# Optimization experiments

Measured on AMD Instinct MI355X. Metric: run time of the kernel, lower is better.

Reference implementation:

```python
import jax, jax.numpy as jnp
import numpy as np

N = 4096          # residues
D = 256           # local feature dim
FACTOR = 2
H = 8             # global heads
DF = D * FACTOR   # 512
DH = DF // H      # 64 per-head dim
NUM_CHAINS = 64
NUM_BATCHES = 8


def index_mean(x, idx, mask, num_segments):
    """Masked segment mean, gathered back to per-element shape.
    x: [N, ...], idx: [N] int, mask: broadcastable to x (0/1)."""
    m = mask.astype(x.dtype)
    xm = x * m
    s = jax.ops.segment_sum(xm, idx, num_segments=num_segments)
    c = jax.ops.segment_sum(jnp.broadcast_to(m, x.shape), idx, num_segments=num_segments)
    mean = s / jnp.maximum(c, 1e-6)
    return mean[idx]


def setup_inputs() -> dict:
    key = jax.random.key(0)
    ks = jax.random.split(key, 12)
    s_in = 1.0 / np.sqrt(D)
    s_mid = 1.0 / np.sqrt(2 * DF)
    return {
        "local": jax.random.normal(ks[0], (N, D), jnp.float32),
        "chain": jax.random.randint(ks[1], (N,), 0, NUM_CHAINS),
        "batch": jax.random.randint(ks[2], (N,), 0, NUM_BATCHES),
        "mask": jax.random.bernoulli(ks[3], 0.9, (N,)),
        "W_key": jax.random.normal(ks[4], (D, DF), jnp.float32) * s_in,
        "b_key": jnp.zeros((DF,), jnp.float32),
        "W_value": jax.random.normal(ks[5], (D, DF), jnp.float32) * s_in,
        "b_value": jnp.zeros((DF,), jnp.float32),
        "W_query": jax.random.normal(ks[6], (D, DF), jnp.float32) * s_in,
        "b_query": jnp.zeros((DF,), jnp.float32),
        "W_bias": jax.random.normal(ks[7], (D, 2 * DF), jnp.float32) * s_in,
        "b_bias": jnp.zeros((2 * DF,), jnp.float32),
        "W_out": jax.random.normal(ks[8], (2 * DF, D), jnp.float32) * s_mid,
    }


def reference(local, chain, batch, mask,
              W_key, b_key, W_value, b_value, W_query, b_query,
              W_bias, b_bias, W_out):
    n = local.shape[0]
    k = jax.nn.gelu(local @ W_key + b_key).reshape(n, H, DH)
    v = (local @ W_value + b_value).reshape(n, H, DH)
    q = jax.nn.gelu(local @ W_query + b_query).reshape(n, H, DH)

    bias = index_mean(local @ W_bias + b_bias, batch, mask[:, None], NUM_BATCHES)

    # outer product key (x) value: [N, H, DH, DH]
    ov = k[:, :, :, None] * v[:, :, None, :]
    m4 = mask[:, None, None, None]
    chain_op = index_mean(ov, chain, m4, NUM_CHAINS)
    batch_op = index_mean(ov, batch, m4, NUM_BATCHES)
    operation = jnp.concatenate((chain_op, batch_op), axis=-2)  # [N, H, 2*DH, DH]

    out = jnp.einsum('bhvk,bhk->bhv', operation, q).reshape(n, -1) + bias
    return out @ W_out
```

## Files before the change

kernel.cpp:

```cpp
#include <hip/hip_runtime.h>
#include <math.h>

#define NN 4096
#define DD 256
#define DFF 512
#define HH 8
#define DHH 64

#define CAP_C 256
#define CAP_B 1024

#define OFF_KB     0
#define OFF_VB     1048576
#define OFF_QB     2097152
#define OFF_ATTNB  3145728
#define OFF_STC    5242880
#define OFF_STB    7340032
#define OFF_LSUM   7602176
#define OFF_BSUM   7604224
#define OFF_CNT    7612416
#define OFF_LOCALB 7612672
#define OFF_WQKVT  8136960
#define OFF_WOUTT  8333568
#define OFF_LISTS  8464640
#define ZERO_BYTES ((OFF_LOCALB - OFF_STB) * 4)

typedef __attribute__((ext_vector_type(8))) short bf16x8;
typedef __attribute__((ext_vector_type(4))) float floatx4;

__device__ __forceinline__ float gelu_f(float x) {
    const float c = 0.7978845608028654f;
    float t = tanhf(c * (x + 0.044715f * x * x * x));
    return 0.5f * x * (1.0f + t);
}

__device__ __forceinline__ unsigned short f2b(float f) {
    union { float f; unsigned int u; } v; v.f = f;
    unsigned int r = (v.u + 0x7FFFu + ((v.u >> 16) & 1u)) >> 16;
    return (unsigned short)r;
}

__device__ __forceinline__ float b2f(unsigned short u) {
    union { unsigned int u; float f; } v; v.u = ((unsigned int)u) << 16;
    return v.f;
}

__global__ __launch_bounds__(256) void prep_kernel(
    const float* __restrict__ local,
    const float* __restrict__ Wk, const float* __restrict__ Wv,
    const float* __restrict__ Wq, const float* __restrict__ Wout,
    unsigned short* __restrict__ localb, unsigned short* __restrict__ Wqkvt,
    unsigned short* __restrict__ Woutt,
    const int* __restrict__ chain, const int* __restrict__ batch,
    const int* __restrict__ mask,
    int* __restrict__ cntc_m, int* __restrict__ cntc_all,
    int* __restrict__ cntb_m, int* __restrict__ cntb_all,
    int* __restrict__ listc_m, int* __restrict__ listc_all,
    int* __restrict__ listb_m, int* __restrict__ listb_all)
{
    const int bid = blockIdx.x, tid = threadIdx.x;
    if (bid < 1024) {
        int base = bid * 1024 + tid * 4;
        float4 v = *(const float4*)(local + base);
        ushort4 o;
        o.x = f2b(v.x); o.y = f2b(v.y); o.z = f2b(v.z); o.w = f2b(v.w);
        *(ushort4*)(localb + base) = o;
    } else if (bid < 1664) {
        int t = bid - 1024;
        const float* src; unsigned short* dst; int R, C, r0, c0;
        if (t < 384) {
            int m = t >> 7, ti = t & 127;
            src = (m == 0) ? Wk : (m == 1) ? Wv : Wq;
            dst = Wqkvt + (size_t)m * 512 * 256;
            R = 256; C = 512;
            r0 = (ti >> 4) * 32; c0 = (ti & 15) * 32;
        } else {
            int ti = t - 384;
            src = Wout; dst = Woutt;
            R = 1024; C = 256;
            r0 = (ti >> 3) * 32; c0 = (ti & 7) * 32;
        }
        __shared__ float Tl[32][33];
        int ty = tid >> 3, tx = tid & 7;
        float4 v = *(const float4*)(src + (size_t)(r0 + ty) * C + c0 + tx * 4);
        Tl[tx * 4 + 0][ty] = v.x;
        Tl[tx * 4 + 1][ty] = v.y;
        Tl[tx * 4 + 2][ty] = v.z;
        Tl[tx * 4 + 3][ty] = v.w;
        __syncthreads();
        int cy = tid >> 3, rx = tid & 7;
        ushort4 o;
        o.x = f2b(Tl[cy][rx * 4 + 0]);
        o.y = f2b(Tl[cy][rx * 4 + 1]);
        o.z = f2b(Tl[cy][rx * 4 + 2]);
        o.w = f2b(Tl[cy][rx * 4 + 3]);
        *(ushort4*)(dst + (size_t)(c0 + cy) * R + r0 + rx * 4) = o;
    } else {
        __shared__ int hc_m[64], hc_all[64], hb_m[8], hb_all[8];
        __shared__ int pc_m[64], pc_all[64], pb_m[8], pb_all[8];
        if (tid < 64) { hc_m[tid] = 0; hc_all[tid] = 0; }
        if (tid < 8)  { hb_m[tid] = 0; hb_all[tid] = 0; }
        __syncthreads();
        int n = (bid - 1664) * 256 + tid;
        int c = chain[n], b = batch[n], m = mask[n];
        int rc_all = atomicAdd(&hc_all[c], 1);
        int rb_all = atomicAdd(&hb_all[b], 1);
        int rc_m = -1, rb_m = -1;
        if (m) {
            rc_m = atomicAdd(&hc_m[c], 1);
            rb_m = atomicAdd(&hb_m[b], 1);
        }
        __syncthreads();
        if (tid < 64) {
            pc_all[tid] = atomicAdd(&cntc_all[tid], hc_all[tid]);
            pc_m[tid]   = atomicAdd(&cntc_m[tid],   hc_m[tid]);
        }
        if (tid < 8) {
            pb_all[tid] = atomicAdd(&cntb_all[tid], hb_all[tid]);
            pb_m[tid]   = atomicAdd(&cntb_m[tid],   hb_m[tid]);
        }
        __syncthreads();
        int ia = pc_all[c] + rc_all;
        if (ia < CAP_C) listc_all[c * CAP_C + ia] = n;
        int ib = pb_all[b] + rb_all;
        if (ib < CAP_B) listb_all[b * CAP_B + ib] = n;
        if (m) {
            int ja = pc_m[c] + rc_m;
            if (ja < CAP_C) listc_m[c * CAP_C + ja] = n;
            int jb = pb_m[b] + rb_m;
            if (jb < CAP_B) listb_m[b * CAP_B + jb] = n;
        }
    }
}

__global__ __launch_bounds__(256) void qkv_plus_kernel(
    const unsigned short* __restrict__ A, const unsigned short* __restrict__ Bt,
    const float* __restrict__ bk, const float* __restrict__ bv,
    const float* __restrict__ bq,
    unsigned short* __restrict__ KVQb,
    const float* __restrict__ local, const int* __restrict__ listb_m,
    const int* __restrict__ cntb_m, float* __restrict__ Lsum)
{
    const int tid = threadIdx.x;
    if (blockIdx.x == 12) {
        const int seg = blockIdx.y >> 2, z = blockIdx.y & 3;
        int c = min(cntb_m[seg], CAP_B);
        int chunk = (c + 3) / 4;
        int r0 = z * chunk, r1 = min(c, r0 + chunk);
        float acc = 0.0f;
        for (int g = r0; g < r1; ++g) {
            int n = listb_m[seg * CAP_B + g];
            acc += local[(size_t)n * DD + tid];
        }
        atomicAdd(&Lsum[seg * DD + tid], acc);
        return;
    }
    const int K = 256;
    __shared__ unsigned short Asl[128][72];
    __shared__ unsigned short Bsl[128][72];
    const int wave = tid >> 6, lane = tid & 63;
    const int kq = lane >> 4, la = lane & 15;
    const int row0 = blockIdx.y * 128, cg0 = blockIdx.x * 128;
    const int wrow = (wave & 1) * 64, wcol = (wave >> 1) * 64;

    floatx4 acc[4][4] = {};
    for (int kk = 0; kk < K; kk += 64) {
#pragma unroll
        for (int t = 0; t < 4; ++t) {
            int idx = tid + t * 256;
            int rr = idx >> 3, kc = (idx & 7) * 8;
            *(float4*)&Asl[rr][kc] = *(const float4*)(A + (size_t)(row0 + rr) * K + kk + kc);
            *(float4*)&Bsl[rr][kc] = *(const float4*)(Bt + (size_t)(cg0 + rr) * K + kk + kc);
        }
        __syncthreads();
#pragma unroll
        for (int ks = 0; ks < 2; ++ks) {
            bf16x8 af[4], bf[4];
#pragma unroll
            for (int t = 0; t < 4; ++t) {
                af[t] = *(const bf16x8*)&Asl[wrow + t * 16 + la][ks * 32 + kq * 8];
                bf[t] = *(const bf16x8*)&Bsl[wcol + t * 16 + la][ks * 32 + kq * 8];
            }
#pragma unroll
            for (int at = 0; at < 4; ++at)
#pragma unroll
                for (int ct = 0; ct < 4; ++ct)
                    acc[at][ct] = __builtin_amdgcn_mfma_f32_16x16x32_bf16(
                        af[at], bf[ct], acc[at][ct], 0, 0, 0);
        }
        __syncthreads();
    }
    const int sel = cg0 >> 9;
    const int do_gelu = (sel != 1);
    const float* bias = (sel == 0) ? bk : (sel == 1) ? bv : bq;
    unsigned short* C = KVQb + (size_t)sel * (NN * DFF);
#pragma unroll
    for (int ct = 0; ct < 4; ++ct) {
        int col = cg0 + wcol + ct * 16 + la;
        int colw = col & 511;
        float bb = bias[colw];
#pragma unroll
        for (int at = 0; at < 4; ++at) {
#pragma unroll
            for (int i = 0; i < 4; ++i) {
                int row = row0 + wrow + at * 16 + kq * 4 + i;
                float o = acc[at][ct][i] + bb;
                if (do_gelu) o = gelu_f(o);
                C[(size_t)row * DFF + colw] = f2b(o);
            }
        }
    }
}

__global__ __launch_bounds__(256) void mid_kernel(
    const unsigned short* __restrict__ Kb, const unsigned short* __restrict__ Vb,
    const int* __restrict__ listc_m, const int* __restrict__ cntc_m,
    float* __restrict__ STc,
    const int* __restrict__ listb_m, const int* __restrict__ cntb_m,
    float* __restrict__ STb,
    const float* __restrict__ Lsum, const float* __restrict__ W_bias,
    float* __restrict__ Bsum)
{
    const int id = blockIdx.x, tid = threadIdx.x;
    if (id >= 1024) {
        int t = id - 1024;
        const int seg = t >> 3, kz = t & 7;
        float4 acc = make_float4(0, 0, 0, 0);
        for (int k = kz * 32; k < kz * 32 + 32; ++k) {
            float l = Lsum[seg * DD + k];
            float4 w = *(const float4*)(W_bias + (size_t)k * 1024 + tid * 4);
            acc.x += l * w.x; acc.y += l * w.y; acc.z += l * w.z; acc.w += l * w.w;
        }
        float* o = Bsum + (size_t)seg * 1024 + tid * 4;
        atomicAdd(o + 0, acc.x);
        atomicAdd(o + 1, acc.y);
        atomicAdd(o + 2, acc.z);
        atomicAdd(o + 3, acc.w);
        return;
    }

    int seg, h, r0, r1, cap;
    const int* list;
    float* ST;
    bool direct;
    if (id < 512) {
        seg = id >> 3; h = id & 7;
        cap = CAP_C; list = listc_m; ST = STc;
        int c = min(cntc_m[seg], CAP_C);
        r0 = 0; r1 = c; direct = true;
    } else {
        int t = id - 512;
        seg = t >> 6; h = (t >> 3) & 7;
        int z = t & 7;
        cap = CAP_B; list = listb_m; ST = STb;
        int c = min(cntb_m[seg], CAP_B);
        int chunk = (c + 7) / 8;
        r0 = z * chunk; r1 = min(c, r0 + chunk); direct = false;
    }

    __shared__ unsigned short Ktl[64][36];
    __shared__ unsigned short Vtl[64][36];
    const int wave = tid >> 6, lane = tid & 63;
    const int la = lane & 15, kq = lane >> 4;

    floatx4 acc[4] = {};
    for (int g = r0; g < r1; g += 32) {
#pragma unroll
        for (int it = 0; it < 2; ++it) {
            int item = tid + it * 256;
            int nl = item & 31, aq = item >> 5;
            int gg = g + nl;
            ushort4 kz4 = make_ushort4(0, 0, 0, 0);
            ushort4 vz4 = make_ushort4(0, 0, 0, 0);
            if (gg < r1) {
                int nn = list[seg * cap + gg];
                kz4 = *(const ushort4*)(Kb + (size_t)nn * DFF + h * DHH + aq * 4);
                vz4 = *(const ushort4*)(Vb + (size_t)nn * DFF + h * DHH + aq * 4);
            }
            Ktl[aq * 4 + 0][nl] = kz4.x;
            Ktl[aq * 4 + 1][nl] = kz4.y;
            Ktl[aq * 4 + 2][nl] = kz4.z;
            Ktl[aq * 4 + 3][nl] = kz4.w;
            Vtl[aq * 4 + 0][nl] = vz4.x;
            Vtl[aq * 4 + 1][nl] = vz4.y;
            Vtl[aq * 4 + 2][nl] = vz4.z;
            Vtl[aq * 4 + 3][nl] = vz4.w;
        }
        __syncthreads();
        bf16x8 a = *(const bf16x8*)&Ktl[wave * 16 + la][kq * 8];
#pragma unroll
        for (int bt = 0; bt < 4; ++bt) {
            bf16x8 b = *(const bf16x8*)&Vtl[bt * 16 + la][kq * 8];
            acc[bt] = __builtin_amdgcn_mfma_f32_16x16x32_bf16(a, b, acc[bt], 0, 0, 0);
        }
        __syncthreads();
    }

    float* outp = ST + (((size_t)seg * HH + h) << 12);
#pragma unroll
    for (int bt = 0; bt < 4; ++bt) {
#pragma unroll
        for (int rg = 0; rg < 4; ++rg) {
            int aa = wave * 16 + kq * 4 + rg;
            int bb = bt * 16 + la;
            if (direct) outp[aa * 64 + bb] = acc[bt][rg];
            else atomicAdd(&outp[aa * 64 + bb], acc[bt][rg]);
        }
    }
}

__global__ __launch_bounds__(256) void einsum_kernel(
    const float* __restrict__ STc, const int* __restrict__ cntc_m,
    const int* __restrict__ listc_all, const int* __restrict__ cntc_all,
    const float* __restrict__ STb, const int* __restrict__ cntb_m,
    const int* __restrict__ listb_all, const int* __restrict__ cntb_all,
    const unsigned short* __restrict__ Qb, const int* __restrict__ batch,
    const float* __restrict__ Bsum, const float* __restrict__ b_bias,
    unsigned short* __restrict__ attnb)
{
    const int id = blockIdx.x, tid = threadIdx.x;
    int seg, h, outoff, cap, r0, r1;
    const float* ST;
    const int* list;
    float scaleS;
    if (id < 512) {
        seg = id >> 3; h = id & 7; outoff = 0;
        ST = STc; list = listc_all; cap = CAP_C;
        scaleS = 1.0f / fmaxf((float)cntc_m[seg], 1e-6f);
        r0 = 0; r1 = min(cntc_all[seg], CAP_C);
    } else {
        int t = id - 512;
        seg = t >> 6; h = (t >> 3) & 7;
        int z = t & 7;
        outoff = 64;
        ST = STb; list = listb_all; cap = CAP_B;
        scaleS = 1.0f / fmaxf((float)cntb_m[seg], 1e-6f);
        int c = min(cntb_all[seg], CAP_B);
        int chunk = (c + 7) / 8;
        r0 = z * chunk; r1 = min(c, r0 + chunk);
    }

    __shared__ unsigned short Sbl[64][72];
    __shared__ unsigned short Qsl[64][72];
    __shared__ float Bf[8][64];
    __shared__ int nrow[64];
    __shared__ int nbb[64];

    const int wave = tid >> 6, lane = tid & 63;
    const int la = lane & 15, kq = lane >> 4;
    const int colbase = h * 128 + outoff;

    const float* Sg = ST + (((size_t)seg * HH + h) << 12);
#pragma unroll
    for (int i = 0; i < 4; ++i) {
        int e = tid + i * 256;
        float4 v = *(const float4*)(Sg + e * 4);
        int a = e >> 4, b = (e & 15) * 4;
        ushort4 o;
        o.x = f2b(v.x * scaleS); o.y = f2b(v.y * scaleS);
        o.z = f2b(v.z * scaleS); o.w = f2b(v.w * scaleS);
        *(ushort4*)&Sbl[a][b] = o;
    }
#pragma unroll
    for (int e = tid; e < 512; e += 256) {
        int bbq = e >> 6, j = e & 63;
        float cm = (float)cntb_m[bbq];
        float inv = 1.0f / fmaxf(cm, 1e-6f);
        int col = colbase + j;
        Bf[bbq][j] = (Bsum[(size_t)bbq * 1024 + col] + cm * b_bias[col]) * inv;
    }
    __syncthreads();

    for (int g = r0; g < r1; g += 64) {
        if (tid < 64) {
            int gg = g + tid;
            int n = (gg < r1) ? list[seg * cap + gg] : -1;
            nrow[tid] = n;
            nbb[tid] = (n >= 0) ? batch[n] : 0;
        }
        __syncthreads();
        {
            int row = tid & 63, pr = tid >> 6;
            int n = nrow[row];
            if (n >= 0) {
#pragma unroll
                for (int it = 0; it < 2; ++it) {
                    int off = (pr + it * 4) * 8;
                    *(float4*)&Qsl[row][off] =
                        *(const float4*)(Qb + (size_t)n * DFF + h * DHH + off);
                }
            }
        }
        __syncthreads();

        floatx4 acc[4] = {};
#pragma unroll
        for (int ks = 0; ks < 2; ++ks) {
            bf16x8 a = *(const bf16x8*)&Qsl[wave * 16 + la][ks * 32 + kq * 8];
#pragma unroll
            for (int ct = 0; ct < 4; ++ct) {
                bf16x8 b = *(const bf16x8*)&Sbl[ct * 16 + la][ks * 32 + kq * 8];
                acc[ct] = __builtin_amdgcn_mfma_f32_16x16x32_bf16(a, b, acc[ct], 0, 0, 0);
            }
        }
#pragma unroll
        for (int ct = 0; ct < 4; ++ct) {
#pragma unroll
            for (int rg = 0; rg < 4; ++rg) {
                int rowl = wave * 16 + kq * 4 + rg;
                float bias = Bf[nbb[rowl]][ct * 16 + la];
                Qsl[rowl][ct * 16 + la] = f2b(acc[ct][rg] + bias);
            }
        }
        __syncthreads();
        {
            int row = tid & 63, pr = tid >> 6;
            int n = nrow[row];
            if (n >= 0) {
#pragma unroll
                for (int it = 0; it < 2; ++it) {
                    int off = (pr + it * 4) * 8;
                    *(float4*)(attnb + (size_t)n * 1024 + colbase + off) =
                        *(const float4*)&Qsl[row][off];
                }
            }
        }
        __syncthreads();
    }
}

__global__ __launch_bounds__(256) void mfma_gemm_final(
    const unsigned short* __restrict__ A, const unsigned short* __restrict__ Bt,
    float* __restrict__ out)
{
    const int K = 1024;
    __shared__ unsigned short Asl[32][136];
    __shared__ unsigned short Bsl[64][136];
    const int tid = threadIdx.x;
    const int wave = tid >> 6, lane = tid & 63;
    const int q = lane >> 4, r = lane & 15;
    const int row0 = blockIdx.y * 32, cg0 = blockIdx.x * 64;
    const int wrow = (wave & 1) * 16, wcol = (wave >> 1) * 32;

    floatx4 acc[2] = {};
    for (int kk = 0; kk < K; kk += 128) {
#pragma unroll
        for (int t = 0; t < 2; ++t) {
            int idx = tid + t * 256;
            int rr = idx >> 4, kc = (idx & 15) * 8;
            *(float4*)&Asl[rr][kc] = *(const float4*)(A + (size_t)(row0 + rr) * K + kk + kc);
        }
#pragma unroll
        for (int t = 0; t < 4; ++t) {
            int idx = tid + t * 256;
            int rr = idx >> 4, kc = (idx & 15) * 8;
            *(float4*)&Bsl[rr][kc] = *(const float4*)(Bt + (size_t)(cg0 + rr) * K + kk + kc);
        }
        __syncthreads();
#pragma unroll
        for (int sub = 0; sub < 4; ++sub) {
            bf16x8 a = *(const bf16x8*)&Asl[wrow + r][sub * 32 + q * 8];
#pragma unroll
            for (int c = 0; c < 2; ++c) {
                bf16x8 b = *(const bf16x8*)&Bsl[wcol + c * 16 + r][sub * 32 + q * 8];
                acc[c] = __builtin_amdgcn_mfma_f32_16x16x32_bf16(a, b, acc[c], 0, 0, 0);
            }
        }
        __syncthreads();
    }
#pragma unroll
    for (int c = 0; c < 2; ++c) {
        int col = cg0 + wcol + c * 16 + r;
#pragma unroll
        for (int i = 0; i < 4; ++i) {
            int row = row0 + wrow + q * 4 + i;
            out[(size_t)row * DD + col] = acc[c][i];
        }
    }
}

extern "C" void kernel_launch(void* const* d_in, const int* in_sizes, int n_in,
                              void* d_out, int out_size, void* d_ws, size_t ws_size,
                              hipStream_t stream)
{
    const float* local   = (const float*)d_in[0];
    const int*   chain   = (const int*)d_in[1];
    const int*   batch   = (const int*)d_in[2];
    const int*   mask    = (const int*)d_in[3];
    const float* W_key   = (const float*)d_in[4];
    const float* b_key   = (const float*)d_in[5];
    const float* W_value = (const float*)d_in[6];
    const float* b_value = (const float*)d_in[7];
    const float* W_query = (const float*)d_in[8];
    const float* b_query = (const float*)d_in[9];
    const float* W_bias  = (const float*)d_in[10];
    const float* b_bias  = (const float*)d_in[11];
    const float* W_out   = (const float*)d_in[12];
    float* out = (float*)d_out;

    float* ws = (float*)d_ws;
    unsigned short* Kb    = (unsigned short*)(ws + OFF_KB);
    unsigned short* Vb    = (unsigned short*)(ws + OFF_VB);
    unsigned short* Qb    = (unsigned short*)(ws + OFF_QB);
    unsigned short* attnb = (unsigned short*)(ws + OFF_ATTNB);
    float* STc    = ws + OFF_STC;
    float* STb    = ws + OFF_STB;
    float* Lsum   = ws + OFF_LSUM;
    float* Bsum   = ws + OFF_BSUM;
    int*   cnt    = (int*)(ws + OFF_CNT);
    unsigned short* localb = (unsigned short*)(ws + OFF_LOCALB);
    unsigned short* Wqkvt  = (unsigned short*)(ws + OFF_WQKVT);
    unsigned short* Woutt  = (unsigned short*)(ws + OFF_WOUTT);
    int* cntc_m   = cnt + 0;
    int* cntc_all = cnt + 64;
    int* cntb_m   = cnt + 128;
    int* cntb_all = cnt + 136;
    int* lists    = (int*)(ws + OFF_LISTS);
    int* listc_m   = lists;
    int* listc_all = listc_m + 64 * CAP_C;
    int* listb_m   = listc_all + 64 * CAP_C;
    int* listb_all = listb_m + 8 * CAP_B;

    dim3 blk(256);

    hipMemsetAsync(ws + OFF_STB, 0, ZERO_BYTES, stream);

    prep_kernel<<<dim3(1680), blk, 0, stream>>>(
        local, W_key, W_value, W_query, W_out, localb, Wqkvt, Woutt,
        chain, batch, mask, cntc_m, cntc_all, cntb_m, cntb_all,
        listc_m, listc_all, listb_m, listb_all);

    qkv_plus_kernel<<<dim3(13, 32), blk, 0, stream>>>(
        localb, Wqkvt, b_key, b_value, b_query, Kb,
        local, listb_m, cntb_m, Lsum);

    mid_kernel<<<dim3(1088), blk, 0, stream>>>(
        Kb, Vb, listc_m, cntc_m, STc, listb_m, cntb_m, STb,
        Lsum, W_bias, Bsum);

    einsum_kernel<<<dim3(1024), blk, 0, stream>>>(
        STc, cntc_m, listc_all, cntc_all, STb, cntb_m, listb_all, cntb_all,
        Qb, batch, Bsum, b_bias, attnb);

    mfma_gemm_final<<<dim3(4, 128), blk, 0, stream>>>(attnb, Woutt, out);
}
```

Before: 158.4 us.

## Fuse all stages into one cooperative persistent kernel with grid syncs

Replaces the memset and five separate kernel launches with a single cooperative mega-kernel. Its phases are separated by grid.sync() and each block loops over work units. The bf16 conversion of `local` is folded into the QKV GEMM's tile loads, and the per-batch local sum is recomputed with a masked scan instead of list-based gathering. This removes launch gaps and the separate conversion pass, but adds grid-wide barriers and limits parallelism to the resident block count, so phases with more than 768 units run in multiple waves.

```diff
diff --git a/kernel.cpp b/kernel.cpp
--- a/kernel.cpp
+++ b/kernel.cpp
@@ -1,12 +1,14 @@
 #include <hip/hip_runtime.h>
+#include <hip/hip_cooperative_groups.h>
 #include <math.h>
+
+namespace cg = cooperative_groups;
 
 #define NN 4096
 #define DD 256
 #define DFF 512
 #define HH 8
 #define DHH 64
-
 #define CAP_C 256
 #define CAP_B 1024
 
@@ -19,11 +21,10 @@
 #define OFF_LSUM   7602176
 #define OFF_BSUM   7604224
 #define OFF_CNT    7612416
-#define OFF_LOCALB 7612672
-#define OFF_WQKVT  8136960
-#define OFF_WOUTT  8333568
-#define OFF_LISTS  8464640
-#define ZERO_BYTES ((OFF_LOCALB - OFF_STB) * 4)
+#define OFF_WQKVT  7612672
+#define OFF_WOUTT  7809280
+#define OFF_LISTS  7940352
+#define ZERO_F4    68160
 
 typedef __attribute__((ext_vector_type(8))) short bf16x8;
 typedef __attribute__((ext_vector_type(4))) float floatx4;
@@ -40,441 +41,427 @@
     return (unsigned short)r;
 }
 
-__device__ __forceinline__ float b2f(unsigned short u) {
-    union { unsigned int u; float f; } v; v.u = ((unsigned int)u) << 16;
-    return v.f;
-}
-
-__global__ __launch_bounds__(256) void prep_kernel(
-    const float* __restrict__ local,
-    const float* __restrict__ Wk, const float* __restrict__ Wv,
-    const float* __restrict__ Wq, const float* __restrict__ Wout,
-    unsigned short* __restrict__ localb, unsigned short* __restrict__ Wqkvt,
-    unsigned short* __restrict__ Woutt,
-    const int* __restrict__ chain, const int* __restrict__ batch,
-    const int* __restrict__ mask,
-    int* __restrict__ cntc_m, int* __restrict__ cntc_all,
-    int* __restrict__ cntb_m, int* __restrict__ cntb_all,
-    int* __restrict__ listc_m, int* __restrict__ listc_all,
-    int* __restrict__ listb_m, int* __restrict__ listb_all)
+__global__ __launch_bounds__(256, 3) void mega_kernel(
+    const float* __restrict__ local, const int* __restrict__ chain,
+    const int* __restrict__ batch, const int* __restrict__ mask,
+    const float* __restrict__ Wk, const float* __restrict__ bk,
+    const float* __restrict__ Wv, const float* __restrict__ bv,
+    const float* __restrict__ Wq, const float* __restrict__ bq,
+    const float* __restrict__ Wbias, const float* __restrict__ bbias,
+    const float* __restrict__ Wout, float* __restrict__ out,
+    float* __restrict__ ws)
 {
-    const int bid = blockIdx.x, tid = threadIdx.x;
-    if (bid < 1024) {
-        int base = bid * 1024 + tid * 4;
-        float4 v = *(const float4*)(local + base);
-        ushort4 o;
-        o.x = f2b(v.x); o.y = f2b(v.y); o.z = f2b(v.z); o.w = f2b(v.w);
-        *(ushort4*)(localb + base) = o;
-    } else if (bid < 1664) {
-        int t = bid - 1024;
-        const float* src; unsigned short* dst; int R, C, r0, c0;
-        if (t < 384) {
-            int m = t >> 7, ti = t & 127;
-            src = (m == 0) ? Wk : (m == 1) ? Wv : Wq;
-            dst = Wqkvt + (size_t)m * 512 * 256;
-            R = 256; C = 512;
-            r0 = (ti >> 4) * 32; c0 = (ti & 15) * 32;
+    __shared__ __align__(16) char smem[36864];
+    const int tid = threadIdx.x;
+    cg::grid_group grid = cg::this_grid();
+
+    unsigned short* Kb    = (unsigned short*)(ws + OFF_KB);
+    unsigned short* Vb    = (unsigned short*)(ws + OFF_VB);
+    unsigned short* Qb    = (unsigned short*)(ws + OFF_QB);
+    unsigned short* attnb = (unsigned short*)(ws + OFF_ATTNB);
+    float* STc  = ws + OFF_STC;
+    float* STb  = ws + OFF_STB;
+    float* Lsum = ws + OFF_LSUM;
+    float* Bsum = ws + OFF_BSUM;
+    int*   cnt  = (int*)(ws + OFF_CNT);
+    unsigned short* Wqkvt = (unsigned short*)(ws + OFF_WQKVT);
+    unsigned short* Woutt = (unsigned short*)(ws + OFF_WOUTT);
+    int* cntc_m   = cnt;
+    int* cntc_all = cnt + 64;
+    int* cntb_m   = cnt + 128;
+    int* cntb_all = cnt + 136;
+    int* listc_m   = (int*)(ws + OFF_LISTS);
+    int* listc_all = listc_m + 64 * CAP_C;
+    int* listb_m   = listc_all + 64 * CAP_C;
+    int* listb_all = listb_m + 8 * CAP_B;
+
+    for (int u = blockIdx.x; u < 672; u += gridDim.x) {
+        if (u < 640) {
+            const float* src; unsigned short* dst; int R, C, r0, c0;
+            if (u < 384) {
+                int m = u >> 7, ti = u & 127;
+                src = (m == 0) ? Wk : (m == 1) ? Wv : Wq;
+                dst = Wqkvt + (size_t)m * 512 * 256;
+                R = 256; C = 512;
+                r0 = (ti >> 4) * 32; c0 = (ti & 15) * 32;
+            } else {
+                int ti = u - 384;
+                src = Wout; dst = Woutt;
+                R = 1024; C = 256;
+                r0 = (ti >> 3) * 32; c0 = (ti & 7) * 32;
+            }
+            float (*Tl)[33] = (float(*)[33])smem;
+            int ty = tid >> 3, tx = tid & 7;
+            float4 v = *(const float4*)(src + (size_t)(r0 + ty) * C + c0 + tx * 4);
+            Tl[tx * 4 + 0][ty] = v.x;
+            Tl[tx * 4 + 1][ty] = v.y;
+            Tl[tx * 4 + 2][ty] = v.z;
+            Tl[tx * 4 + 3][ty] = v.w;
+            __syncthreads();
+            ushort4 o;
+            o.x = f2b(Tl[ty][tx * 4 + 0]);
+            o.y = f2b(Tl[ty][tx * 4 + 1]);
+            o.z = f2b(Tl[ty][tx * 4 + 2]);
+            o.w = f2b(Tl[ty][tx * 4 + 3]);
+            *(ushort4*)(dst + (size_t)(c0 + ty) * R + r0 + tx * 4) = o;
+            __syncthreads();
         } else {
-            int ti = t - 384;
-            src = Wout; dst = Woutt;
-            R = 1024; C = 256;
-            r0 = (ti >> 3) * 32; c0 = (ti & 7) * 32;
-        }
-        __shared__ float Tl[32][33];
-        int ty = tid >> 3, tx = tid & 7;
-        float4 v = *(const float4*)(src + (size_t)(r0 + ty) * C + c0 + tx * 4);
-        Tl[tx * 4 + 0][ty] = v.x;
-        Tl[tx * 4 + 1][ty] = v.y;
-        Tl[tx * 4 + 2][ty] = v.z;
-        Tl[tx * 4 + 3][ty] = v.w;
+            int z = u - 640;
+            float4 z4 = make_float4(0.f, 0.f, 0.f, 0.f);
+            float* base = ws + OFF_STB;
+            for (int idx = z * 256 + tid; idx < ZERO_F4; idx += 32 * 256)
+                *(float4*)(base + (size_t)idx * 4) = z4;
+        }
+    }
+    grid.sync();
+
+    for (int u = blockIdx.x; u < 416; u += gridDim.x) {
+        if (u < 384) {
+            typedef unsigned short (*t72)[72];
+            t72 Asl = (t72)smem;
+            t72 Bsl = (t72)(smem + 18432);
+            const int wave = tid >> 6, lane = tid & 63;
+            const int kq = lane >> 4, la = lane & 15;
+            const int cx = u % 12, ry = u / 12;
+            const int row0 = ry * 128, cg0 = cx * 128;
+            const int wrow = (wave & 1) * 64, wcol = (wave >> 1) * 64;
+
+            floatx4 acc[4][4] = {};
+            for (int kk = 0; kk < 256; kk += 64) {
+#pragma unroll
+                for (int t = 0; t < 4; ++t) {
+                    int idx = tid + t * 256;
+                    int rr = idx >> 3, kc = (idx & 7) * 8;
+                    const float* ap = local + (size_t)(row0 + rr) * DD + kk + kc;
+                    float4 a0 = *(const float4*)(ap);
+                    float4 a1 = *(const float4*)(ap + 4);
+                    ushort4 p0, p1;
+                    p0.x = f2b(a0.x); p0.y = f2b(a0.y); p0.z = f2b(a0.z); p0.w = f2b(a0.w);
+                    p1.x = f2b(a1.x); p1.y = f2b(a1.y); p1.z = f2b(a1.z); p1.w = f2b(a1.w);
+                    *(ushort4*)&Asl[rr][kc] = p0;
+                    *(ushort4*)&Asl[rr][kc + 4] = p1;
+                    *(float4*)&Bsl[rr][kc] =
+                        *(const float4*)(Wqkvt + (size_t)(cg0 + rr) * DD + kk + kc);
+                }
+                __syncthreads();
+#pragma unroll
+                for (int ks = 0; ks < 2; ++ks) {
+                    bf16x8 af[4], bf[4];
+#pragma unroll
+                    for (int t = 0; t < 4; ++t) {
+                        af[t] = *(const bf16x8*)&Asl[wrow + t * 16 + la][ks * 32 + kq * 8];
+                        bf[t] = *(const bf16x8*)&Bsl[wcol + t * 16 + la][ks * 32 + kq * 8];
+                    }
+#pragma unroll
+                    for (int at = 0; at < 4; ++at)
+#pragma unroll
+                        for (int ct = 0; ct < 4; ++ct)
+                            acc[at][ct] = __builtin_amdgcn_mfma_f32_16x16x32_bf16(
+                                af[at], bf[ct], acc[at][ct], 0, 0, 0);
+                }
+                __syncthreads();
+            }
+            const int sel = cg0 >> 9;
+            const int do_gelu = (sel != 1);
+            const float* bias = (sel == 0) ? bk : (sel == 1) ? bv : bq;
+            unsigned short* C = Kb + (size_t)sel * (NN * DFF);
+#pragma unroll
+            for (int ct = 0; ct < 4; ++ct) {
+                int colw = (cg0 + wcol + ct * 16 + la) & 511;
+                float bb = bias[colw];
+#pragma unroll
+                for (int at = 0; at < 4; ++at)
+#pragma unroll
+                    for (int i = 0; i < 4; ++i) {
+                        int row = row0 + wrow + at * 16 + kq * 4 + i;
+                        float o = acc[at][ct][i] + bb;
+                        if (do_gelu) o = gelu_f(o);
+                        C[(size_t)row * DFF + colw] = f2b(o);
+                    }
+            }
+        } else if (u < 400) {
+            int* sh = (int*)smem;
+            int* hc_m = sh;        int* hc_all = sh + 64;
+            int* hb_m = sh + 128;  int* hb_all = sh + 136;
+            int* pc_m = sh + 144;  int* pc_all = sh + 208;
+            int* pb_m = sh + 272;  int* pb_all = sh + 280;
+            if (tid < 64) { hc_m[tid] = 0; hc_all[tid] = 0; }
+            if (tid < 8)  { hb_m[tid] = 0; hb_all[tid] = 0; }
+            __syncthreads();
+            int n = (u - 384) * 256 + tid;
+            int c = chain[n], b = batch[n], m = mask[n];
+            int rc_all = atomicAdd(&hc_all[c], 1);
+            int rb_all = atomicAdd(&hb_all[b], 1);
+            int rc_m = -1, rb_m = -1;
+            if (m) { rc_m = atomicAdd(&hc_m[c], 1); rb_m = atomicAdd(&hb_m[b], 1); }
+            __syncthreads();
+            if (tid < 64) {
+                pc_all[tid] = atomicAdd(&cntc_all[tid], hc_all[tid]);
+                pc_m[tid]   = atomicAdd(&cntc_m[tid],   hc_m[tid]);
+            }
+            if (tid < 8) {
+                pb_all[tid] = atomicAdd(&cntb_all[tid], hb_all[tid]);
+                pb_m[tid]   = atomicAdd(&cntb_m[tid],   hb_m[tid]);
+            }
+            __syncthreads();
+            int ia = pc_all[c] + rc_all; if (ia < CAP_C) listc_all[c * CAP_C + ia] = n;
+            int ib = pb_all[b] + rb_all; if (ib < CAP_B) listb_all[b * CAP_B + ib] = n;
+            if (m) {
+                int ja = pc_m[c] + rc_m; if (ja < CAP_C) listc_m[c * CAP_C + ja] = n;
+                int jb = pb_m[b] + rb_m; if (jb < CAP_B) listb_m[b * CAP_B + jb] = n;
+            }
+            __syncthreads();
+        } else {
+            int i = u - 400;
+            float accl[8] = {};
+            int n0 = i * 256;
+            for (int r = 0; r < 256; ++r) {
+                int n = n0 + r;
+                float v = local[(size_t)n * DD + tid];
+                int bb = batch[n];
+                float vm = mask[n] ? v : 0.0f;
+#pragma unroll
+                for (int b = 0; b < 8; ++b)
+                    accl[b] += (bb == b) ? vm : 0.0f;
+            }
+#pragma unroll
+            for (int b = 0; b < 8; ++b)
+                atomicAdd(&Lsum[b * DD + tid], accl[b]);
+        }
+    }
+    grid.sync();
+
+    for (int u = blockIdx.x; u < 1088; u += gridDim.x) {
+        if (u >= 1024) {
+            int t = u - 1024;
+            int seg = t >> 3, kz = t & 7;
+            float4 a4 = make_float4(0, 0, 0, 0);
+            for (int k = kz * 32; k < kz * 32 + 32; ++k) {
+                float l = Lsum[seg * DD + k];
+                float4 w = *(const float4*)(Wbias + (size_t)k * 1024 + tid * 4);
+                a4.x += l * w.x; a4.y += l * w.y; a4.z += l * w.z; a4.w += l * w.w;
+            }
+            float* o = Bsum + (size_t)seg * 1024 + tid * 4;
+            atomicAdd(o + 0, a4.x); atomicAdd(o + 1, a4.y);
+            atomicAdd(o + 2, a4.z); atomicAdd(o + 3, a4.w);
+        } else {
+            int seg, h, r0, r1, cap;
+            const int* list; float* ST; bool direct;
+            if (u < 512) {
+                seg = u >> 3; h = u & 7;
+                cap = CAP_C; list = listc_m; ST = STc;
+                r0 = 0; r1 = min(cntc_m[seg], CAP_C); direct = true;
+            } else {
+                int t = u - 512;
+                seg = t >> 6; h = (t >> 3) & 7;
+                int z = t & 7;
+                cap = CAP_B; list = listb_m; ST = STb;
+                int c = min(cntb_m[seg], CAP_B);
+                int chunk = (c + 7) / 8;
+                r0 = z * chunk; r1 = min(c, r0 + chunk); direct = false;
+            }
+            typedef unsigned short (*t36)[36];
+            t36 Ktl = (t36)smem;
+            t36 Vtl = (t36)(smem + 4608);
+            const int wave = tid >> 6, lane = tid & 63;
+            const int la = lane & 15, kq = lane >> 4;
+            floatx4 acc4[4] = {};
+            for (int g = r0; g < r1; g += 32) {
+#pragma unroll
+                for (int it = 0; it < 2; ++it) {
+                    int item = tid + it * 256;
+                    int nl = item & 31, aq = item >> 5;
+                    int gg = g + nl;
+                    ushort4 kz4 = make_ushort4(0, 0, 0, 0);
+                    ushort4 vz4 = make_ushort4(0, 0, 0, 0);
+                    if (gg < r1) {
+                        int nn = list[seg * cap + gg];
+                        kz4 = *(const ushort4*)(Kb + (size_t)nn * DFF + h * DHH + aq * 4);
+                        vz4 = *(const ushort4*)(Vb + (size_t)nn * DFF + h * DHH + aq * 4);
+                    }
+                    Ktl[aq * 4 + 0][nl] = kz4.x; Ktl[aq * 4 + 1][nl] = kz4.y;
+                    Ktl[aq * 4 + 2][nl] = kz4.z; Ktl[aq * 4 + 3][nl] = kz4.w;
+                    Vtl[aq * 4 + 0][nl] = vz4.x; Vtl[aq * 4 + 1][nl] = vz4.y;
+                    Vtl[aq * 4 + 2][nl] = vz4.z; Vtl[aq * 4 + 3][nl] = vz4.w;
+                }
+                __syncthreads();
+                bf16x8 a = *(const bf16x8*)&Ktl[wave * 16 + la][kq * 8];
+#pragma unroll
+                for (int bt = 0; bt < 4; ++bt) {
+                    bf16x8 b = *(const bf16x8*)&Vtl[bt * 16 + la][kq * 8];
+                    acc4[bt] = __builtin_amdgcn_mfma_f32_16x16x32_bf16(a, b, acc4[bt], 0, 0, 0);
+                }
+                __syncthreads();
+            }
+            float* outp = ST + (((size_t)seg * HH + h) << 12);
+#pragma unroll
+            for (int bt = 0; bt < 4; ++bt)
+#pragma unroll
+                for (int rg = 0; rg < 4; ++rg) {
+                    int aa = wave * 16 + kq * 4 + rg;
+                    int bb2 = bt * 16 + la;
+                    if (direct) outp[aa * 64 + bb2] = acc4[bt][rg];
+                    else atomicAdd(&outp[aa * 64 + bb2], acc4[bt][rg]);
+                }
+        }
+    }
+    grid.sync();
+
+    for (int u = blockIdx.x; u < 1024; u += gridDim.x) {
+        int seg, h, outoff, cap, r0, r1;
+        const float* ST; const int* list; float scaleS;
+        if (u < 512) {
+            seg = u >> 3; h = u & 7; outoff = 0;
+            ST = STc; list = listc_all; cap = CAP_C;
+            scaleS = 1.0f / fmaxf((float)cntc_m[seg], 1e-6f);
+            r0 = 0; r1 = min(cntc_all[seg], CAP_C);
+        } else {
+            int t = u - 512;
+            seg = t >> 6; h = (t >> 3) & 7;
+            int z = t & 7;
+            outoff = 64;
+            ST = STb; list = listb_all; cap = CAP_B;
+            scaleS = 1.0f / fmaxf((float)cntb_m[seg], 1e-6f);
+            int c = min(cntb_all[seg], CAP_B);
+            int chunk = (c + 7) / 8;
+            r0 = z * chunk; r1 = min(c, r0 + chunk);
+        }
+        typedef unsigned short (*t72)[72];
+        t72 Sbl = (t72)smem;
+        t72 Qsl = (t72)(smem + 9216);
+        float (*Bf)[64] = (float(*)[64])(smem + 18432);
+        int* nrow = (int*)(smem + 20480);
+        int* nbb  = (int*)(smem + 20736);
+
+        const int wave = tid >> 6, lane = tid & 63;
+        const int la = lane & 15, kq = lane >> 4;
+        const int colbase = h * 128 + outoff;
+
+        const float* Sg = ST + (((size_t)seg * HH + h) << 12);
+#pragma unroll
+        for (int i = 0; i < 4; ++i) {
+            int e = tid + i * 256;
+            float4 v = *(const float4*)(Sg + (size_t)e * 4);
+            int a = e >> 4, b = (e & 15) * 4;
+            ushort4 o;
+            o.x = f2b(v.x * scaleS); o.y = f2b(v.y * scaleS);
+            o.z = f2b(v.z * scaleS); o.w = f2b(v.w * scaleS);
+            *(ushort4*)&Sbl[a][b] = o;
+        }
+#pragma unroll
+        for (int e = tid; e < 512; e += 256) {
+            int bbq = e >> 6, j = e & 63;
+            float cm = (float)cntb_m[bbq];
+            float inv = 1.0f / fmaxf(cm, 1e-6f);
+            int col = colbase + j;
+            Bf[bbq][j] = (Bsum[(size_t)bbq * 1024 + col] + cm * bbias[col]) * inv;
+        }
         __syncthreads();
-        int cy = tid >> 3, rx = tid & 7;
-        ushort4 o;
-        o.x = f2b(Tl[cy][rx * 4 + 0]);
-        o.y = f2b(Tl[cy][rx * 4 + 1]);
-        o.z = f2b(Tl[cy][rx * 4 + 2]);
-        o.w = f2b(Tl[cy][rx * 4 + 3]);
-        *(ushort4*)(dst + (size_t)(c0 + cy) * R + r0 + rx * 4) = o;
-    } else {
-        __shared__ int hc_m[64], hc_all[64], hb_m[8], hb_all[8];
-        __shared__ int pc_m[64], pc_all[64], pb_m[8], pb_all[8];
-        if (tid < 64) { hc_m[tid] = 0; hc_all[tid] = 0; }
-        if (tid < 8)  { hb_m[tid] = 0; hb_all[tid] = 0; }
-        __syncthreads();
-        int n = (bid - 1664) * 256 + tid;
-        int c = chain[n], b = batch[n], m = mask[n];
-        int rc_all = atomicAdd(&hc_all[c], 1);
-        int rb_all = atomicAdd(&hb_all[b], 1);
-        int rc_m = -1, rb_m = -1;
-        if (m) {
-            rc_m = atomicAdd(&hc_m[c], 1);
-            rb_m = atomicAdd(&hb_m[b], 1);
-        }
-        __syncthreads();
-        if (tid < 64) {
-            pc_all[tid] = atomicAdd(&cntc_all[tid], hc_all[tid]);
-            pc_m[tid]   = atomicAdd(&cntc_m[tid],   hc_m[tid]);
-        }
-        if (tid < 8) {
-            pb_all[tid] = atomicAdd(&cntb_all[tid], hb_all[tid]);
-            pb_m[tid]   = atomicAdd(&cntb_m[tid],   hb_m[tid]);
-        }
-        __syncthreads();
-        int ia = pc_all[c] + rc_all;
-        if (ia < CAP_C) listc_all[c * CAP_C + ia] = n;
-        int ib = pb_all[b] + rb_all;
-        if (ib < CAP_B) listb_all[b * CAP_B + ib] = n;
-        if (m) {
-            int ja = pc_m[c] + rc_m;
-            if (ja < CAP_C) listc_m[c * CAP_C + ja] = n;
-            int jb = pb_m[b] + rb_m;
-            if (jb < CAP_B) listb_m[b * CAP_B + jb] = n;
+
+        for (int g = r0; g < r1; g += 64) {
+            if (tid < 64) {
+                int gg = g + tid;
+                int n = (gg < r1) ? list[seg * cap + gg] : -1;
+                nrow[tid] = n;
+                nbb[tid] = (n >= 0) ? batch[n] : 0;
+            }
+            __syncthreads();
+            {
+                int row = tid & 63, pr = tid >> 6;
+                int n = nrow[row];
+                if (n >= 0) {
+#pragma unroll
+                    for (int it = 0; it < 2; ++it) {
+                        int off = (pr + it * 4) * 8;
+                        *(float4*)&Qsl[row][off] =
+                            *(const float4*)(Qb + (size_t)n * DFF + h * DHH + off);
+                    }
+                }
+            }
+            __syncthreads();
+
+            floatx4 acc[4] = {};
+#pragma unroll
+            for (int ks = 0; ks < 2; ++ks) {
+                bf16x8 a = *(const bf16x8*)&Qsl[wave * 16 + la][ks * 32 + kq * 8];
+#pragma unroll
+                for (int ct = 0; ct < 4; ++ct) {
+                    bf16x8 b = *(const bf16x8*)&Sbl[ct * 16 + la][ks * 32 + kq * 8];
+                    acc[ct] = __builtin_amdgcn_mfma_f32_16x16x32_bf16(a, b, acc[ct], 0, 0, 0);
+                }
+            }
+#pragma unroll
+            for (int ct = 0; ct < 4; ++ct)
+#pragma unroll
+                for (int rg = 0; rg < 4; ++rg) {
+                    int rowl = wave * 16 + kq * 4 + rg;
+                    float bias = Bf[nbb[rowl]][ct * 16 + la];
+                    Qsl[rowl][ct * 16 + la] = f2b(acc[ct][rg] + bias);
+                }
+            __syncthreads();
+            {
+                int row = tid & 63, pr = tid >> 6;
+                int n = nrow[row];
+                if (n >= 0) {
+#pragma unroll
+                    for (int it = 0; it < 2; ++it) {
+                        int off = (pr + it * 4) * 8;
+                        *(float4*)(attnb + (size_t)n * 1024 + colbase + off) =
+                            *(const float4*)&Qsl[row][off];
+                    }
+                }
+            }
+            __syncthreads();
         }
     }
-}
-
-__global__ __launch_bounds__(256) void qkv_plus_kernel(
-    const unsigned short* __restrict__ A, const unsigned short* __restrict__ Bt,
-    const float* __restrict__ bk, const float* __restrict__ bv,
-    const float* __restrict__ bq,
-    unsigned short* __restrict__ KVQb,
-    const float* __restrict__ local, const int* __restrict__ listb_m,
-    const int* __restrict__ cntb_m, float* __restrict__ Lsum)
-{
-    const int tid = threadIdx.x;
-    if (blockIdx.x == 12) {
-        const int seg = blockIdx.y >> 2, z = blockIdx.y & 3;
-        int c = min(cntb_m[seg], CAP_B);
-        int chunk = (c + 3) / 4;
-        int r0 = z * chunk, r1 = min(c, r0 + chunk);
-        float acc = 0.0f;
-        for (int g = r0; g < r1; ++g) {
-            int n = listb_m[seg * CAP_B + g];
-            acc += local[(size_t)n * DD + tid];
-        }
-        atomicAdd(&Lsum[seg * DD + tid], acc);
-        return;
-    }
-    const int K = 256;
-    __shared__ unsigned short Asl[128][72];
-    __shared__ unsigned short Bsl[128][72];
-    const int wave = tid >> 6, lane = tid & 63;
-    const int kq = lane >> 4, la = lane & 15;
-    const int row0 = blockIdx.y * 128, cg0 = blockIdx.x * 128;
-    const int wrow = (wave & 1) * 64, wcol = (wave >> 1) * 64;
-
-    floatx4 acc[4][4] = {};
-    for (int kk = 0; kk < K; kk += 64) {
-#pragma unroll
-        for (int t = 0; t < 4; ++t) {
-            int idx = tid + t * 256;
-            int rr = idx >> 3, kc = (idx & 7) * 8;
-            *(float4*)&Asl[rr][kc] = *(const float4*)(A + (size_t)(row0 + rr) * K + kk + kc);
-            *(float4*)&Bsl[rr][kc] = *(const float4*)(Bt + (size_t)(cg0 + rr) * K + kk + kc);
-        }
-        __syncthreads();
-#pragma unroll
-        for (int ks = 0; ks < 2; ++ks) {
-            bf16x8 af[4], bf[4];
+    grid.sync();
+
+    for (int u = blockIdx.x; u < 512; u += gridDim.x) {
+        const int K = 1024;
+        typedef unsigned short (*t136)[136];
+        t136 Asl = (t136)smem;
+        t136 Bsl = (t136)(smem + 8704);
+        const int wave = tid >> 6, lane = tid & 63;
+        const int q = lane >> 4, r = lane & 15;
+        const int row0 = (u >> 2) * 32, cg0 = (u & 3) * 64;
+        const int wrow = (wave & 1) * 16, wcol = (wave >> 1) * 32;
+
+        floatx4 acc[2] = {};
+        for (int kk = 0; kk < K; kk += 128) {
+#pragma unroll
+            for (int t = 0; t < 2; ++t) {
+                int idx = tid + t * 256;
+                int rr = idx >> 4, kc = (idx & 15) * 8;
+                *(float4*)&Asl[rr][kc] =
+                    *(const float4*)(attnb + (size_t)(row0 + rr) * K + kk + kc);
+            }
 #pragma unroll
             for (int t = 0; t < 4; ++t) {
-                af[t] = *(const bf16x8*)&Asl[wrow + t * 16 + la][ks * 32 + kq * 8];
-                bf[t] = *(const bf16x8*)&Bsl[wcol + t * 16 + la][ks * 32 + kq * 8];
-            }
-#pragma unroll
-            for (int at = 0; at < 4; ++at)
-#pragma unroll
-                for (int ct = 0; ct < 4; ++ct)
-                    acc[at][ct] = __builtin_amdgcn_mfma_f32_16x16x32_bf16(
-                        af[at], bf[ct], acc[at][ct], 0, 0, 0);
-        }
-        __syncthreads();
-    }
-    const int sel = cg0 >> 9;
-    const int do_gelu = (sel != 1);
-    const float* bias = (sel == 0) ? bk : (sel == 1) ? bv : bq;
-    unsigned short* C = KVQb + (size_t)sel * (NN * DFF);
-#pragma unroll
-    for (int ct = 0; ct < 4; ++ct) {
-        int col = cg0 + wcol + ct * 16 + la;
-        int colw = col & 511;
-        float bb = bias[colw];
-#pragma unroll
-        for (int at = 0; at < 4; ++at) {
+                int idx = tid + t * 256;
+                int rr = idx >> 4, kc = (idx & 15) * 8;
+                *(float4*)&Bsl[rr][kc] =
+                    *(const float4*)(Woutt + (size_t)(cg0 + rr) * K + kk + kc);
+            }
+            __syncthreads();
+#pragma unroll
+            for (int sub = 0; sub < 4; ++sub) {
+                bf16x8 a = *(const bf16x8*)&Asl[wrow + r][sub * 32 + q * 8];
+#pragma unroll
+                for (int c = 0; c < 2; ++c) {
+                    bf16x8 b = *(const bf16x8*)&Bsl[wcol + c * 16 + r][sub * 32 + q * 8];
+                    acc[c] = __builtin_amdgcn_mfma_f32_16x16x32_bf16(a, b, acc[c], 0, 0, 0);
+                }
+            }
+            __syncthreads();
+        }
+#pragma unroll
+        for (int c = 0; c < 2; ++c) {
+            int col = cg0 + wcol + c * 16 + r;
 #pragma unroll
             for (int i = 0; i < 4; ++i) {
-                int row = row0 + wrow + at * 16 + kq * 4 + i;
-                float o = acc[at][ct][i] + bb;
-                if (do_gelu) o = gelu_f(o);
-                C[(size_t)row * DFF + colw] = f2b(o);
-            }
-        }
-    }
-}
-
-__global__ __launch_bounds__(256) void mid_kernel(
-    const unsigned short* __restrict__ Kb, const unsigned short* __restrict__ Vb,
-    const int* __restrict__ listc_m, const int* __restrict__ cntc_m,
-    float* __restrict__ STc,
-    const int* __restrict__ listb_m, const int* __restrict__ cntb_m,
-    float* __restrict__ STb,
-    const float* __restrict__ Lsum, const float* __restrict__ W_bias,
-    float* __restrict__ Bsum)
-{
-    const int id = blockIdx.x, tid = threadIdx.x;
-    if (id >= 1024) {
-        int t = id - 1024;
-        const int seg = t >> 3, kz = t & 7;
-        float4 acc = make_float4(0, 0, 0, 0);
-        for (int k = kz * 32; k < kz * 32 + 32; ++k) {
-            float l = Lsum[seg * DD + k];
-            float4 w = *(const float4*)(W_bias + (size_t)k * 1024 + tid * 4);
-            acc.x += l * w.x; acc.y += l * w.y; acc.z += l * w.z; acc.w += l * w.w;
-        }
-        float* o = Bsum + (size_t)seg * 1024 + tid * 4;
-        atomicAdd(o + 0, acc.x);
-        atomicAdd(o + 1, acc.y);
-        atomicAdd(o + 2, acc.z);
-        atomicAdd(o + 3, acc.w);
-        return;
-    }
-
-    int seg, h, r0, r1, cap;
-    const int* list;
-    float* ST;
-    bool direct;
-    if (id < 512) {
-        seg = id >> 3; h = id & 7;
-        cap = CAP_C; list = listc_m; ST = STc;
-        int c = min(cntc_m[seg], CAP_C);
-        r0 = 0; r1 = c; direct = true;
-    } else {
-        int t = id - 512;
-        seg = t >> 6; h = (t >> 3) & 7;
-        int z = t & 7;
-        cap = CAP_B; list = listb_m; ST = STb;
-        int c = min(cntb_m[seg], CAP_B);
-        int chunk = (c + 7) / 8;
-        r0 = z * chunk; r1 = min(c, r0 + chunk); direct = false;
-    }
-
-    __shared__ unsigned short Ktl[64][36];
-    __shared__ unsigned short Vtl[64][36];
-    const int wave = tid >> 6, lane = tid & 63;
-    const int la = lane & 15, kq = lane >> 4;
-
-    floatx4 acc[4] = {};
-    for (int g = r0; g < r1; g += 32) {
-#pragma unroll
-        for (int it = 0; it < 2; ++it) {
-            int item = tid + it * 256;
-            int nl = item & 31, aq = item >> 5;
-            int gg = g + nl;
-            ushort4 kz4 = make_ushort4(0, 0, 0, 0);
-            ushort4 vz4 = make_ushort4(0, 0, 0, 0);
-            if (gg < r1) {
-                int nn = list[seg * cap + gg];
-                kz4 = *(const ushort4*)(Kb + (size_t)nn * DFF + h * DHH + aq * 4);
-                vz4 = *(const ushort4*)(Vb + (size_t)nn * DFF + h * DHH + aq * 4);
-            }
-            Ktl[aq * 4 + 0][nl] = kz4.x;
-            Ktl[aq * 4 + 1][nl] = kz4.y;
-            Ktl[aq * 4 + 2][nl] = kz4.z;
-            Ktl[aq * 4 + 3][nl] = kz4.w;
-            Vtl[aq * 4 + 0][nl] = vz4.x;
-            Vtl[aq * 4 + 1][nl] = vz4.y;
-            Vtl[aq * 4 + 2][nl] = vz4.z;
-            Vtl[aq * 4 + 3][nl] = vz4.w;
-        }
-        __syncthreads();
-        bf16x8 a = *(const bf16x8*)&Ktl[wave * 16 + la][kq * 8];
-#pragma unroll
-        for (int bt = 0; bt < 4; ++bt) {
-            bf16x8 b = *(const bf16x8*)&Vtl[bt * 16 + la][kq * 8];
-            acc[bt] = __builtin_amdgcn_mfma_f32_16x16x32_bf16(a, b, acc[bt], 0, 0, 0);
-        }
-        __syncthreads();
-    }
-
-    float* outp = ST + (((size_t)seg * HH + h) << 12);
-#pragma unroll
-    for (int bt = 0; bt < 4; ++bt) {
-#pragma unroll
-        for (int rg = 0; rg < 4; ++rg) {
-            int aa = wave * 16 + kq * 4 + rg;
-            int bb = bt * 16 + la;
-            if (direct) outp[aa * 64 + bb] = acc[bt][rg];
-            else atomicAdd(&outp[aa * 64 + bb], acc[bt][rg]);
-        }
-    }
-}
-
-__global__ __launch_bounds__(256) void einsum_kernel(
-    const float* __restrict__ STc, const int* __restrict__ cntc_m,
-    const int* __restrict__ listc_all, const int* __restrict__ cntc_all,
-    const float* __restrict__ STb, const int* __restrict__ cntb_m,
-    const int* __restrict__ listb_all, const int* __restrict__ cntb_all,
-    const unsigned short* __restrict__ Qb, const int* __restrict__ batch,
-    const float* __restrict__ Bsum, const float* __restrict__ b_bias,
-    unsigned short* __restrict__ attnb)
-{
-    const int id = blockIdx.x, tid = threadIdx.x;
-    int seg, h, outoff, cap, r0, r1;
-    const float* ST;
-    const int* list;
-    float scaleS;
-    if (id < 512) {
-        seg = id >> 3; h = id & 7; outoff = 0;
-        ST = STc; list = listc_all; cap = CAP_C;
-        scaleS = 1.0f / fmaxf((float)cntc_m[seg], 1e-6f);
-        r0 = 0; r1 = min(cntc_all[seg], CAP_C);
-    } else {
-        int t = id - 512;
-        seg = t >> 6; h = (t >> 3) & 7;
-        int z = t & 7;
-        outoff = 64;
-        ST = STb; list = listb_all; cap = CAP_B;
-        scaleS = 1.0f / fmaxf((float)cntb_m[seg], 1e-6f);
-        int c = min(cntb_all[seg], CAP_B);
-        int chunk = (c + 7) / 8;
-        r0 = z * chunk; r1 = min(c, r0 + chunk);
-    }
-
-    __shared__ unsigned short Sbl[64][72];
-    __shared__ unsigned short Qsl[64][72];
-    __shared__ float Bf[8][64];
-    __shared__ int nrow[64];
-    __shared__ int nbb[64];
-
-    const int wave = tid >> 6, lane = tid & 63;
-    const int la = lane & 15, kq = lane >> 4;
-    const int colbase = h * 128 + outoff;
-
-    const float* Sg = ST + (((size_t)seg * HH + h) << 12);
-#pragma unroll
-    for (int i = 0; i < 4; ++i) {
-        int e = tid + i * 256;
-        float4 v = *(const float4*)(Sg + e * 4);
-        int a = e >> 4, b = (e & 15) * 4;
-        ushort4 o;
-        o.x = f2b(v.x * scaleS); o.y = f2b(v.y * scaleS);
-        o.z = f2b(v.z * scaleS); o.w = f2b(v.w * scaleS);
-        *(ushort4*)&Sbl[a][b] = o;
-    }
-#pragma unroll
-    for (int e = tid; e < 512; e += 256) {
-        int bbq = e >> 6, j = e & 63;
-        float cm = (float)cntb_m[bbq];
-        float inv = 1.0f / fmaxf(cm, 1e-6f);
-        int col = colbase + j;
-        Bf[bbq][j] = (Bsum[(size_t)bbq * 1024 + col] + cm * b_bias[col]) * inv;
-    }
-    __syncthreads();
-
-    for (int g = r0; g < r1; g += 64) {
-        if (tid < 64) {
-            int gg = g + tid;
-            int n = (gg < r1) ? list[seg * cap + gg] : -1;
-            nrow[tid] = n;
-            nbb[tid] = (n >= 0) ? batch[n] : 0;
-        }
-        __syncthreads();
-        {
-            int row = tid & 63, pr = tid >> 6;
-            int n = nrow[row];
-            if (n >= 0) {
-#pragma unroll
-                for (int it = 0; it < 2; ++it) {
-                    int off = (pr + it * 4) * 8;
-                    *(float4*)&Qsl[row][off] =
-                        *(const float4*)(Qb + (size_t)n * DFF + h * DHH + off);
-                }
-            }
-        }
-        __syncthreads();
-
-        floatx4 acc[4] = {};
-#pragma unroll
-        for (int ks = 0; ks < 2; ++ks) {
-            bf16x8 a = *(const bf16x8*)&Qsl[wave * 16 + la][ks * 32 + kq * 8];
-#pragma unroll
-            for (int ct = 0; ct < 4; ++ct) {
-                bf16x8 b = *(const bf16x8*)&Sbl[ct * 16 + la][ks * 32 + kq * 8];
-                acc[ct] = __builtin_amdgcn_mfma_f32_16x16x32_bf16(a, b, acc[ct], 0, 0, 0);
-            }
-        }
-#pragma unroll
-        for (int ct = 0; ct < 4; ++ct) {
-#pragma unroll
-            for (int rg = 0; rg < 4; ++rg) {
-                int rowl = wave * 16 + kq * 4 + rg;
-                float bias = Bf[nbb[rowl]][ct * 16 + la];
-                Qsl[rowl][ct * 16 + la] = f2b(acc[ct][rg] + bias);
-            }
-        }
-        __syncthreads();
-        {
-            int row = tid & 63, pr = tid >> 6;
-            int n = nrow[row];
-            if (n >= 0) {
-#pragma unroll
-                for (int it = 0; it < 2; ++it) {
-                    int off = (pr + it * 4) * 8;
-                    *(float4*)(attnb + (size_t)n * 1024 + colbase + off) =
-                        *(const float4*)&Qsl[row][off];
-                }
-            }
-        }
-        __syncthreads();
-    }
-}
-
-__global__ __launch_bounds__(256) void mfma_gemm_final(
-    const unsigned short* __restrict__ A, const unsigned short* __restrict__ Bt,
-    float* __restrict__ out)
-{
-    const int K = 1024;
-    __shared__ unsigned short Asl[32][136];
-    __shared__ unsigned short Bsl[64][136];
-    const int tid = threadIdx.x;
-    const int wave = tid >> 6, lane = tid & 63;
-    const int q = lane >> 4, r = lane & 15;
-    const int row0 = blockIdx.y * 32, cg0 = blockIdx.x * 64;
-    const int wrow = (wave & 1) * 16, wcol = (wave >> 1) * 32;
-
-    floatx4 acc[2] = {};
-    for (int kk = 0; kk < K; kk += 128) {
-#pragma unroll
-        for (int t = 0; t < 2; ++t) {
-            int idx = tid + t * 256;
-            int rr = idx >> 4, kc = (idx & 15) * 8;
-            *(float4*)&Asl[rr][kc] = *(const float4*)(A + (size_t)(row0 + rr) * K + kk + kc);
-        }
-#pragma unroll
-        for (int t = 0; t < 4; ++t) {
-            int idx = tid + t * 256;
-            int rr = idx >> 4, kc = (idx & 15) * 8;
-            *(float4*)&Bsl[rr][kc] = *(const float4*)(Bt + (size_t)(cg0 + rr) * K + kk + kc);
-        }
-        __syncthreads();
-#pragma unroll
-        for (int sub = 0; sub < 4; ++sub) {
-            bf16x8 a = *(const bf16x8*)&Asl[wrow + r][sub * 32 + q * 8];
-#pragma unroll
-            for (int c = 0; c < 2; ++c) {
-                bf16x8 b = *(const bf16x8*)&Bsl[wcol + c * 16 + r][sub * 32 + q * 8];
-                acc[c] = __builtin_amdgcn_mfma_f32_16x16x32_bf16(a, b, acc[c], 0, 0, 0);
-            }
-        }
-        __syncthreads();
-    }
-#pragma unroll
-    for (int c = 0; c < 2; ++c) {
-        int col = cg0 + wcol + c * 16 + r;
-#pragma unroll
-        for (int i = 0; i < 4; ++i) {
-            int row = row0 + wrow + q * 4 + i;
-            out[(size_t)row * DD + col] = acc[c][i];
+                int row = row0 + wrow + q * 4 + i;
+                out[(size_t)row * DD + col] = acc[c][i];
+            }
         }
     }
 }
@@ -497,50 +484,18 @@
     const float* b_bias  = (const float*)d_in[11];
     const float* W_out   = (const float*)d_in[12];
     float* out = (float*)d_out;
-
-    float* ws = (float*)d_ws;
-    unsigned short* Kb    = (unsigned short*)(ws + OFF_KB);
-    unsigned short* Vb    = (unsigned short*)(ws + OFF_VB);
-    unsigned short* Qb    = (unsigned short*)(ws + OFF_QB);
-    unsigned short* attnb = (unsigned short*)(ws + OFF_ATTNB);
-    float* STc    = ws + OFF_STC;
-    float* STb    = ws + OFF_STB;
-    float* Lsum   = ws + OFF_LSUM;
-    float* Bsum   = ws + OFF_BSUM;
-    int*   cnt    = (int*)(ws + OFF_CNT);
-    unsigned short* localb = (unsigned short*)(ws + OFF_LOCALB);
-    unsigned short* Wqkvt  = (unsigned short*)(ws + OFF_WQKVT);
-    unsigned short* Woutt  = (unsigned short*)(ws + OFF_WOUTT);
-    int* cntc_m   = cnt + 0;
-    int* cntc_all = cnt + 64;
-    int* cntb_m   = cnt + 128;
-    int* cntb_all = cnt + 136;
-    int* lists    = (int*)(ws + OFF_LISTS);
-    int* listc_m   = lists;
-    int* listc_all = listc_m + 64 * CAP_C;
-    int* listb_m   = listc_all + 64 * CAP_C;
-    int* listb_all = listb_m + 8 * CAP_B;
-
-    dim3 blk(256);
-
-    hipMemsetAsync(ws + OFF_STB, 0, ZERO_BYTES, stream);
-
-    prep_kernel<<<dim3(1680), blk, 0, stream>>>(
-        local, W_key, W_value, W_query, W_out, localb, Wqkvt, Woutt,
-        chain, batch, mask, cntc_m, cntc_all, cntb_m, cntb_all,
-        listc_m, listc_all, listb_m, listb_all);
-
-    qkv_plus_kernel<<<dim3(13, 32), blk, 0, stream>>>(
-        localb, Wqkvt, b_key, b_value, b_query, Kb,
-        local, listb_m, cntb_m, Lsum);
-
-    mid_kernel<<<dim3(1088), blk, 0, stream>>>(
-        Kb, Vb, listc_m, cntc_m, STc, listb_m, cntb_m, STb,
-        Lsum, W_bias, Bsum);
-
-    einsum_kernel<<<dim3(1024), blk, 0, stream>>>(
-        STc, cntc_m, listc_all, cntc_all, STb, cntb_m, listb_all, cntb_all,
-        Qb, batch, Bsum, b_bias, attnb);
-
-    mfma_gemm_final<<<dim3(4, 128), blk, 0, stream>>>(attnb, Woutt, out);
+    float* ws  = (float*)d_ws;
+
+    int occ = 0;
+    if (hipOccupancyMaxActiveBlocksPerMultiprocessor(&occ, mega_kernel, 256, 0) != hipSuccess || occ < 1)
+        occ = 1;
+    int grid = occ * 256;
+    if (grid > 768) grid = 768;
+
+    void* kargs[] = {
+        (void*)&local, (void*)&chain, (void*)&batch, (void*)&mask,
+        (void*)&W_key, (void*)&b_key, (void*)&W_value, (void*)&b_value,
+        (void*)&W_query, (void*)&b_query, (void*)&W_bias, (void*)&b_bias,
+        (void*)&W_out, (void*)&out, (void*)&ws };
+    hipLaunchCooperativeKernel((void*)mega_kernel, dim3(grid), dim3(256), kargs, 0, stream);
 }
```

Result: slower. 369.5 us (+133.2%).
